# Kernel tuning notes

Hardware: AMD Instinct MI355X
Metric: run time of the kernel (lower is better)

## Reference

```python
import jax, jax.numpy as jnp
import numpy as np
from jax import lax

# Per-tensor power-of-two scales (ScalingImplType.CONST / POWER_OF_TWO in Brevitas)
S_ACT8 = 2.0 ** -4   # 8-bit signed input quant scale
S_ACT4 = 2.0 ** -1   # 4-bit signed input quant scale
S_W = 2.0 ** -2      # per-tensor weight quant scale
S_RELU = 2.0 ** -2   # 4-bit unsigned QuantReLU scale


def fq(x, scale, qmin, qmax):
    # fake-quant with straight-through estimator (STE)
    q = jnp.clip(jnp.round(x / scale), qmin, qmax) * scale
    return x + lax.stop_gradient(q - x)


def fq_signed(x, scale, bits):
    return fq(x, scale, -(2 ** (bits - 1)), 2 ** (bits - 1) - 1)


def fq_uint(x, scale, bits):
    return fq(x, scale, 0, 2 ** bits - 1)


def qconv(x, w, in_bits, w_bits, s_in, stride=1, padding=0, groups=1):
    xq = fq_signed(x, s_in, in_bits)
    wq = fq_signed(w, S_W, w_bits)
    return lax.conv_general_dilated(
        xq, wq, (stride, stride), [(padding, padding)] * 2,
        feature_group_count=groups,
        dimension_numbers=('NCHW', 'OIHW', 'NCHW'))


def maxpool(x, k, s):
    return lax.reduce_window(x, -jnp.inf, lax.max,
                             (1, 1, k, k), (1, 1, s, s), 'VALID')


def dwsep(x, dw, pw):
    c = x.shape[1]
    x = qconv(x, dw, 4, 4, S_ACT4, padding=1, groups=c)  # depthwise 3x3
    x = qconv(x, pw, 4, 4, S_ACT4)                       # pointwise 1x1
    return x


def qrelu4(x):
    return fq_uint(jax.nn.relu(x), S_RELU, 4)


def setup_inputs() -> dict:
    key = jax.random.key(0)
    ks = jax.random.split(key, 10)
    B = 1024
    mk = lambda k, shp, sc=0.5: jax.random.normal(k, shp, jnp.float32) * sc
    return {
        'x': jax.random.normal(ks[0], (B, 3, 32, 32), jnp.float32),
        'w0': mk(ks[1], (3, 3, 1, 1)),
        'dw1': mk(ks[2], (3, 1, 3, 3)),
        'pw1': mk(ks[3], (32, 3, 1, 1)),
        'dw2': mk(ks[4], (32, 1, 3, 3)),
        'pw2': mk(ks[5], (64, 32, 1, 1)),
        'dw3': mk(ks[6], (64, 1, 3, 3)),
        'pw3': mk(ks[7], (128, 64, 1, 1)),
        'wc1': mk(ks[8], (256, 128, 1, 1)),
        'wc2': mk(ks[9], (10, 256, 1, 1)),
    }


def reference(x, w0, dw1, pw1, dw2, pw2, dw3, pw3, wc1, wc2):
    # features
    h = qconv(x, w0, 8, 8, S_ACT8)            # 1x1, 3->3, 8-bit
    h = dwsep(h, dw1, pw1)                    # 3->32, 32x32
    h = qrelu4(h)
    h = maxpool(h, 2, 2)                      # 16x16
    h = dwsep(h, dw2, pw2)                    # 32->64
    h = qrelu4(h)
    h = maxpool(h, 2, 2)                      # 8x8
    h = dwsep(h, dw3, pw3)                    # 64->128
    h = qrelu4(h)
    h = maxpool(h, 8, 1)                      # 1x1
    # classifier
    h = qconv(h, wc1, 4, 4, S_ACT4)           # 128->256
    h = qrelu4(h)
    h = qconv(h, wc2, 4, 4, S_ACT4)           # 256->10
    h = fq_signed(h, S_ACT8, 8)               # output quant int8
    return h
```

## Files before the change

### kernel.cpp

```cpp
#include <hip/hip_runtime.h>

#define W0i   0
#define DW1i  9
#define PW1i  36
#define DW2i  132
#define DW3i  420
#define PW2p  996
#define PW3p  1508
#define WC1p  3556
#define WC2p  11748
#define WTOT  12388

__device__ __forceinline__ int iclamp(int v, int lo, int hi) {
  return v < lo ? lo : (v > hi ? hi : v);
}

__device__ __forceinline__ int rne4(int a) {
  return (a + 1 + ((a >> 2) & 1)) >> 2;
}
__device__ __forceinline__ int rne32(int a) {
  return (a + 15 + ((a >> 5) & 1)) >> 5;
}

__device__ __forceinline__ int dot4(int a, int b, int c) {
#if defined(__has_builtin)
#if __has_builtin(__builtin_amdgcn_sdot4)
  return __builtin_amdgcn_sdot4(a, b, c, false);
#else
  c += ((a << 24) >> 24) * ((b << 24) >> 24);
  c += ((a << 16) >> 24) * ((b << 16) >> 24);
  c += ((a <<  8) >> 24) * ((b <<  8) >> 24);
  c += (a >> 24) * (b >> 24);
  return c;
#endif
#else
  c += ((a << 24) >> 24) * ((b << 24) >> 24);
  c += ((a << 16) >> 24) * ((b << 16) >> 24);
  c += ((a <<  8) >> 24) * ((b <<  8) >> 24);
  c += (a >> 24) * (b >> 24);
  return c;
#endif
}

__device__ __forceinline__ int alignb(int hi, int lo, int sh) {
#if defined(__has_builtin)
#if __has_builtin(__builtin_amdgcn_alignbyte)
  return __builtin_amdgcn_alignbyte(hi, lo, sh);
#else
  return (int)(((((unsigned long long)(unsigned)hi) << 32) |
                (unsigned)lo) >> (8 * sh));
#endif
#else
  return (int)(((((unsigned long long)(unsigned)hi) << 32) |
                (unsigned)lo) >> (8 * sh));
#endif
}

__device__ __forceinline__ int pack3(int a, int b, int c) {
  return (a & 0xff) | ((b & 0xff) << 8) | ((c & 0xff) << 16);
}

__global__ __launch_bounds__(256) void prep_weights(
    const float* __restrict__ w0,  const float* __restrict__ dw1,
    const float* __restrict__ pw1, const float* __restrict__ dw2,
    const float* __restrict__ pw2, const float* __restrict__ dw3,
    const float* __restrict__ pw3, const float* __restrict__ wc1,
    const float* __restrict__ wc2, int* __restrict__ ws) {
  int t = blockIdx.x * blockDim.x + threadIdx.x;
  if (t >= WTOT) return;
  if (t < PW2p) {
    float w; int lo = -8, hi = 7;
    if (t < DW1i)      { w = w0[t];        lo = -128; hi = 127; }
    else if (t < PW1i)   w = dw1[t - DW1i];
    else if (t < DW2i)   w = pw1[t - PW1i];
    else if (t < DW3i)   w = dw2[t - DW2i];
    else                 w = dw3[t - DW3i];
    ws[t] = iclamp((int)rintf(w * 4.f), lo, hi);
  } else {
    const float* src;
    if (t < WC1p) {
      if (t < PW3p) src = pw2 + (t - PW2p) * 4;
      else          src = pw3 + (t - PW3p) * 4;
    } else {
      if (t < WC2p) src = wc1 + (t - WC1p) * 4;
      else          src = wc2 + (t - WC2p) * 4;
    }
    int p = 0;
#pragma unroll
    for (int b = 0; b < 4; b++) {
      int c = iclamp((int)rintf(src[b] * 4.f), -8, 7);
      p |= (c & 0xff) << (8 * b);
    }
    ws[t] = p;
  }
}

__global__ __launch_bounds__(256, 4) void fused_net(
    const float* __restrict__ x,
    const int*   __restrict__ wq,
    float* __restrict__ out)
{
  const int img = blockIdx.x;
  const int tid = threadIdx.x;

  __shared__ __align__(16) int bufAi[2384];
  __shared__ __align__(16) int bufBi[2592];
  __shared__ int s_red[256];

  {
    const float* xim = x + (size_t)img * 3072;
    const int p4 = tid * 4;
    float4 v0 = *(const float4*)(xim + p4);
    float4 v1 = *(const float4*)(xim + 1024 + p4);
    float4 v2 = *(const float4*)(xim + 2048 + p4);
    int w[9];
#pragma unroll
    for (int i = 0; i < 9; i++) w[i] = wq[W0i + i];
#define Q8(v) iclamp((int)rintf((v) * 16.f), -128, 127)
    int a0[4] = {Q8(v0.x), Q8(v0.y), Q8(v0.z), Q8(v0.w)};
    int a1[4] = {Q8(v1.x), Q8(v1.y), Q8(v1.z), Q8(v1.w)};
    int a2[4] = {Q8(v2.x), Q8(v2.y), Q8(v2.z), Q8(v2.w)};
#undef Q8
#pragma unroll
    for (int o = 0; o < 3; o++) {
      int pk = 0;
#pragma unroll
      for (int j = 0; j < 4; j++) {
        int s = a0[j] * w[o * 3] + a1[j] * w[o * 3 + 1] + a2[j] * w[o * 3 + 2];
        pk |= (iclamp(rne32(s), -8, 7) & 0xff) << (8 * j);
      }
      bufAi[o * 256 + tid] = pk;
    }
  }
  __syncthreads();

  {
    const int y = tid >> 3, q = tid & 7;
#pragma unroll
    for (int c = 0; c < 3; c++) {
      int wr[3];
#pragma unroll
      for (int r = 0; r < 3; r++)
        wr[r] = pack3(wq[DW1i + c * 9 + r * 3], wq[DW1i + c * 9 + r * 3 + 1],
                      wq[DW1i + c * 9 + r * 3 + 2]);
      const int* ap = bufAi + c * 256;
      int acc0 = 0, acc1 = 0, acc2 = 0, acc3 = 0;
#pragma unroll
      for (int ky = 0; ky < 3; ky++) {
        int yy = y + ky - 1;
        if (yy < 0 || yy > 31) continue;
        int base = yy * 8 + q;
        int dC = ap[base];
        int dL = q ? ap[base - 1] : 0;
        int dR = (q < 7) ? ap[base + 1] : 0;
        int w = wr[ky];
        acc0 = dot4(alignb(dC, dL, 3), w, acc0);
        acc1 = dot4(dC, w, acc1);
        acc2 = dot4(alignb(dR, dC, 1), w, acc2);
        acc3 = dot4(alignb(dR, dC, 2), w, acc3);
      }
      int pk = (iclamp(rne4(acc0), -8, 7) & 0xff) |
               ((iclamp(rne4(acc1), -8, 7) & 0xff) << 8) |
               ((iclamp(rne4(acc2), -8, 7) & 0xff) << 16) |
               ((iclamp(rne4(acc3), -8, 7) & 0xff) << 24);
      bufBi[c * 256 + tid] = pk;
    }
  }
  __syncthreads();

  {
    const int py = tid >> 4, px = tid & 15;
    const signed char* bB = (const signed char*)bufBi;
    int a[4];
#pragma unroll
    for (int d = 0; d < 4; d++) {
      int sp = (2 * py + (d >> 1)) * 32 + 2 * px + (d & 1);
      a[d] = pack3(bB[sp], bB[1024 + sp], bB[2048 + sp]);
    }
#pragma unroll
    for (int it = 0; it < 8; it++) {
      int pk = 0;
#pragma unroll
      for (int j = 0; j < 4; j++) {
        int o = it * 4 + j;
        int wpk = pack3(wq[PW1i + o * 3], wq[PW1i + o * 3 + 1],
                        wq[PW1i + o * 3 + 2]);
        int m0 = dot4(a[0], wpk, 0), m1 = dot4(a[1], wpk, 0);
        int m2 = dot4(a[2], wpk, 0), m3 = dot4(a[3], wpk, 0);
        int mx = max(max(m0, m1), max(m2, m3));
        pk |= iclamp(rne4(mx), 0, 7) << (8 * j);
      }
      bufAi[py * 149 + px * 9 + it] = pk;
    }
  }
  __syncthreads();

  for (int it2 = 0; it2 < 2; it2++) {
    int idx = tid + 256 * it2;
    int cq = __builtin_amdgcn_readfirstlane(idx >> 6);
    int s = idx & 63;
    int y = s >> 2, x0 = (s & 3) << 2;
    int wk[9][4];
#pragma unroll
    for (int t9 = 0; t9 < 9; t9++)
#pragma unroll
      for (int cc = 0; cc < 4; cc++)
        wk[t9][cc] = wq[DW2i + (cq * 4 + cc) * 9 + t9];
    int acc[4][4] = {};
#pragma unroll
    for (int ky = 0; ky < 3; ky++) {
      int yy = y + ky - 1;
      if (yy < 0 || yy > 15) continue;
      int rb = yy * 149 + cq;
      int rd[6];
      rd[0] = (x0 > 0) ? bufAi[rb + (x0 - 1) * 9] : 0;
      rd[1] = bufAi[rb + x0 * 9];
      rd[2] = bufAi[rb + (x0 + 1) * 9];
      rd[3] = bufAi[rb + (x0 + 2) * 9];
      rd[4] = bufAi[rb + (x0 + 3) * 9];
      rd[5] = (x0 < 12) ? bufAi[rb + (x0 + 4) * 9] : 0;
      int e[6][4];
#pragma unroll
      for (int k = 0; k < 6; k++)
#pragma unroll
        for (int cc = 0; cc < 4; cc++) e[k][cc] = (rd[k] >> (8 * cc)) & 0xf;
#pragma unroll
      for (int j = 0; j < 4; j++)
#pragma unroll
        for (int kx = 0; kx < 3; kx++)
#pragma unroll
          for (int cc = 0; cc < 4; cc++)
            acc[j][cc] += e[j + kx][cc] * wk[ky * 3 + kx][cc];
    }
#pragma unroll
    for (int j = 0; j < 4; j++) {
      int pk = 0;
#pragma unroll
      for (int cc = 0; cc < 4; cc++)
        pk |= (iclamp(rne4(acc[j][cc]), -8, 7) & 0xff) << (8 * cc);
      bufBi[y * 162 + (x0 + j) * 10 + cq] = pk;
    }
  }
  __syncthreads();

  {
    int oq = tid & 15;
    int4 w4[4][2];
#pragma unroll
    for (int j = 0; j < 4; j++) {
      const int4* wp = (const int4*)(wq + PW2p + (oq * 4 + j) * 8);
      w4[j][0] = wp[0]; w4[j][1] = wp[1];
    }
    for (int it = 0; it < 4; it++) {
      int pp = (tid >> 4) + 16 * it;
      int py = pp >> 3, px = pp & 7;
      int mx[4] = {-1000000, -1000000, -1000000, -1000000};
#pragma unroll
      for (int d = 0; d < 4; d++) {
        int sy = 2 * py + (d >> 1), sx = 2 * px + (d & 1);
        const int2* ap = (const int2*)(bufBi + sy * 162 + sx * 10);
        int2 A0 = ap[0], A1 = ap[1], A2 = ap[2], A3 = ap[3];
#pragma unroll
        for (int j = 0; j < 4; j++) {
          int acc = dot4(A0.x, w4[j][0].x, 0);
          acc = dot4(A0.y, w4[j][0].y, acc);
          acc = dot4(A1.x, w4[j][0].z, acc);
          acc = dot4(A1.y, w4[j][0].w, acc);
          acc = dot4(A2.x, w4[j][1].x, acc);
          acc = dot4(A2.y, w4[j][1].y, acc);
          acc = dot4(A3.x, w4[j][1].z, acc);
          acc = dot4(A3.y, w4[j][1].w, acc);
          mx[j] = mx[j] > acc ? mx[j] : acc;
        }
      }
      int pk = 0;
#pragma unroll
      for (int j = 0; j < 4; j++)
        pk |= iclamp(rne4(mx[j]), 0, 7) << (8 * j);
      bufAi[py * 137 + px * 17 + oq] = pk;
    }
  }
  __syncthreads();

  {
    int cq2 = tid >> 4;
    int s = tid & 15;
    int y = s >> 1, x0 = (s & 1) << 2;
    int wk[9][4];
#pragma unroll
    for (int t9 = 0; t9 < 9; t9++)
#pragma unroll
      for (int cc = 0; cc < 4; cc++)
        wk[t9][cc] = wq[DW3i + (cq2 * 4 + cc) * 9 + t9];
    int acc[4][4] = {};
#pragma unroll
    for (int ky = 0; ky < 3; ky++) {
      int yy = y + ky - 1;
      if (yy < 0 || yy > 7) continue;
      int rb = yy * 137 + cq2;
      int rd[6];
      rd[0] = (x0 == 4) ? bufAi[rb + (x0 - 1) * 17] : 0;
      rd[1] = bufAi[rb + x0 * 17];
      rd[2] = bufAi[rb + (x0 + 1) * 17];
      rd[3] = bufAi[rb + (x0 + 2) * 17];
      rd[4] = bufAi[rb + (x0 + 3) * 17];
      rd[5] = (x0 == 0) ? bufAi[rb + (x0 + 4) * 17] : 0;
      int e[6][4];
#pragma unroll
      for (int k = 0; k < 6; k++)
#pragma unroll
        for (int cc = 0; cc < 4; cc++) e[k][cc] = (rd[k] >> (8 * cc)) & 0xf;
#pragma unroll
      for (int j = 0; j < 4; j++)
#pragma unroll
        for (int kx = 0; kx < 3; kx++)
#pragma unroll
          for (int cc = 0; cc < 4; cc++)
            acc[j][cc] += e[j + kx][cc] * wk[ky * 3 + kx][cc];
    }
#pragma unroll
    for (int j = 0; j < 4; j++) {
      int pk = 0;
#pragma unroll
      for (int cc = 0; cc < 4; cc++)
        pk |= (iclamp(rne4(acc[j][cc]), -8, 7) & 0xff) << (8 * cc);
      bufBi[y * 164 + (x0 + j) * 20 + cq2] = pk;
    }
  }
  __syncthreads();

  {
    int o = tid >> 1, half = tid & 1;
    const int4* wp = (const int4*)(wq + PW3p + o * 16);
    int4 w0v = wp[0], w1v = wp[1], w2v = wp[2], w3v = wp[3];
    int mx = -1000000;
    for (int k = 0; k < 32; k++) {
      int sp = half + 2 * k;
      int py = sp >> 3, px = sp & 7;
      const int4* ap = (const int4*)(bufBi + py * 164 + px * 20);
      int4 A0 = ap[0], A1 = ap[1], A2 = ap[2], A3 = ap[3];
      int acc = dot4(A0.x, w0v.x, 0);
      acc = dot4(A0.y, w0v.y, acc); acc = dot4(A0.z, w0v.z, acc);
      acc = dot4(A0.w, w0v.w, acc);
      acc = dot4(A1.x, w1v.x, acc); acc = dot4(A1.y, w1v.y, acc);
      acc = dot4(A1.z, w1v.z, acc); acc = dot4(A1.w, w1v.w, acc);
      acc = dot4(A2.x, w2v.x, acc); acc = dot4(A2.y, w2v.y, acc);
      acc = dot4(A2.z, w2v.z, acc); acc = dot4(A2.w, w2v.w, acc);
      acc = dot4(A3.x, w3v.x, acc); acc = dot4(A3.y, w3v.y, acc);
      acc = dot4(A3.z, w3v.z, acc); acc = dot4(A3.w, w3v.w, acc);
      mx = mx > acc ? mx : acc;
    }
    s_red[tid] = mx;
  }
  __syncthreads();
  if (tid < 128) {
    int mm = s_red[2 * tid] > s_red[2 * tid + 1] ? s_red[2 * tid]
                                                 : s_red[2 * tid + 1];
    ((signed char*)bufAi)[tid] = (signed char)iclamp(rne4(mm), 0, 7);
  }
  __syncthreads();

  {
    const int4* wp = (const int4*)(wq + WC1p + tid * 32);
    const int4* mp = (const int4*)bufAi;
    int acc = 0;
#pragma unroll
    for (int rI = 0; rI < 8; rI++) {
      int4 a = mp[rI]; int4 w = wp[rI];
      acc = dot4(a.x, w.x, acc); acc = dot4(a.y, w.y, acc);
      acc = dot4(a.z, w.z, acc); acc = dot4(a.w, w.w, acc);
    }
    ((signed char*)bufBi)[tid] = (signed char)iclamp(rne4(acc), 0, 7);
  }
  __syncthreads();

  if (tid < 80) {
    int k = tid >> 3, j = tid & 7;
    const int4* wp = (const int4*)(wq + WC2p + k * 64 + j * 8);
    int4 w0v = wp[0], w1v = wp[1];
    const int4* ap = (const int4*)bufBi;
    int4 A0 = ap[j * 2], A1 = ap[j * 2 + 1];
    int acc = dot4(A0.x, w0v.x, 0);
    acc = dot4(A0.y, w0v.y, acc); acc = dot4(A0.z, w0v.z, acc);
    acc = dot4(A0.w, w0v.w, acc);
    acc = dot4(A1.x, w1v.x, acc); acc = dot4(A1.y, w1v.y, acc);
    acc = dot4(A1.z, w1v.z, acc); acc = dot4(A1.w, w1v.w, acc);
    s_red[tid] = acc;
  }
  __syncthreads();
  if (tid < 10) {
    int acc = 0;
#pragma unroll
    for (int j = 0; j < 8; j++) acc += s_red[tid * 8 + j];
    int code = iclamp(2 * acc, -128, 127);
    out[(size_t)img * 10 + tid] = (float)code * 0.0625f;
  }
}

extern "C" void kernel_launch(void* const* d_in, const int* in_sizes, int n_in,
                              void* d_out, int out_size, void* d_ws, size_t ws_size,
                              hipStream_t stream) {
  const float* x   = (const float*)d_in[0];
  const float* w0  = (const float*)d_in[1];
  const float* dw1 = (const float*)d_in[2];
  const float* pw1 = (const float*)d_in[3];
  const float* dw2 = (const float*)d_in[4];
  const float* pw2 = (const float*)d_in[5];
  const float* dw3 = (const float*)d_in[6];
  const float* pw3 = (const float*)d_in[7];
  const float* wc1 = (const float*)d_in[8];
  const float* wc2 = (const float*)d_in[9];
  int*   wsq = (int*)d_ws;
  float* out = (float*)d_out;

  prep_weights<<<(WTOT + 255) / 256, 256, 0, stream>>>(
      w0, dw1, pw1, dw2, pw2, dw3, pw3, wc1, wc2, wsq);
  fused_net<<<1024, 256, 0, stream>>>(x, wsq, out);
}
```

Baseline: 105.9 us.

## Use MFMA int8 matrix instructions for pointwise convs pw2 and pw3

Replaces the sdot4-based pointwise 1x1 convolutions in stages 2 and 3 with __builtin_amdgcn_mfma_i32_16x16x32_i8. The prep kernel adds pre-swizzled weight fragments in MFMA B-operand layout, and activations are regathered in shared memory so each 2x2 maxpool window falls inside one MFMA tile. Pooling then becomes a max over accumulator lanes plus cross-lane shuffles. This cuts the VALU dot-product work, at the cost of an extra LDS gather pass, more shared memory and different buffer ping-ponging that could cause bank conflicts or reduce occupancy.

```diff
diff --git a/kernel.cpp b/kernel.cpp
--- a/kernel.cpp
+++ b/kernel.cpp
@@ -1,4 +1,6 @@
 #include <hip/hip_runtime.h>
+
+typedef int v4i __attribute__((ext_vector_type(4)));
 
 #define W0i   0
 #define DW1i  9
@@ -9,12 +11,13 @@
 #define PW3p  1508
 #define WC1p  3556
 #define WC2p  11748
-#define WTOT  12388
+#define PW2Fb 12388
+#define PW3Fb 12900
+#define WTOT  14948
 
 __device__ __forceinline__ int iclamp(int v, int lo, int hi) {
   return v < lo ? lo : (v > hi ? hi : v);
 }
-
 __device__ __forceinline__ int rne4(int a) {
   return (a + 1 + ((a >> 2) & 1)) >> 2;
 }
@@ -23,8 +26,7 @@
 }
 
 __device__ __forceinline__ int dot4(int a, int b, int c) {
-#if defined(__has_builtin)
-#if __has_builtin(__builtin_amdgcn_sdot4)
+#if defined(__has_builtin) && __has_builtin(__builtin_amdgcn_sdot4)
   return __builtin_amdgcn_sdot4(a, b, c, false);
 #else
   c += ((a << 24) >> 24) * ((b << 24) >> 24);
@@ -33,23 +35,11 @@
   c += (a >> 24) * (b >> 24);
   return c;
 #endif
-#else
-  c += ((a << 24) >> 24) * ((b << 24) >> 24);
-  c += ((a << 16) >> 24) * ((b << 16) >> 24);
-  c += ((a <<  8) >> 24) * ((b <<  8) >> 24);
-  c += (a >> 24) * (b >> 24);
-  return c;
-#endif
 }
 
 __device__ __forceinline__ int alignb(int hi, int lo, int sh) {
-#if defined(__has_builtin)
-#if __has_builtin(__builtin_amdgcn_alignbyte)
+#if defined(__has_builtin) && __has_builtin(__builtin_amdgcn_alignbyte)
   return __builtin_amdgcn_alignbyte(hi, lo, sh);
-#else
-  return (int)(((((unsigned long long)(unsigned)hi) << 32) |
-                (unsigned)lo) >> (8 * sh));
-#endif
 #else
   return (int)(((((unsigned long long)(unsigned)hi) << 32) |
                 (unsigned)lo) >> (8 * sh));
@@ -76,7 +66,7 @@
     else if (t < DW3i)   w = dw2[t - DW2i];
     else                 w = dw3[t - DW3i];
     ws[t] = iclamp((int)rintf(w * 4.f), lo, hi);
-  } else {
+  } else if (t < PW2Fb) {
     const float* src;
     if (t < WC1p) {
       if (t < PW3p) src = pw2 + (t - PW2p) * 4;
@@ -92,6 +82,31 @@
       p |= (c & 0xff) << (8 * b);
     }
     ws[t] = p;
+  } else if (t < PW3Fb) {
+    int i = t - PW2Fb;
+    int nt = i >> 7, r = i & 127, lane = r >> 1, dw = r & 1;
+    int n = nt * 16 + (lane & 15);
+    int kb = (lane >> 4) * 8 + dw * 4;
+    int p = 0;
+#pragma unroll
+    for (int b = 0; b < 4; b++) {
+      int c = iclamp((int)rintf(pw2[n * 32 + kb + b] * 4.f), -8, 7);
+      p |= (c & 0xff) << (8 * b);
+    }
+    ws[t] = p;
+  } else {
+    int i = t - PW3Fb;
+    int g = i >> 7, r = i & 127, lane = r >> 1, dw = r & 1;
+    int nt = g >> 1, kh = g & 1;
+    int n = nt * 16 + (lane & 15);
+    int kb = kh * 32 + (lane >> 4) * 8 + dw * 4;
+    int p = 0;
+#pragma unroll
+    for (int b = 0; b < 4; b++) {
+      int c = iclamp((int)rintf(pw3[n * 64 + kb + b] * 4.f), -8, 7);
+      p |= (c & 0xff) << (8 * b);
+    }
+    ws[t] = p;
   }
 }
 
@@ -103,7 +118,7 @@
   const int img = blockIdx.x;
   const int tid = threadIdx.x;
 
-  __shared__ __align__(16) int bufAi[2384];
+  __shared__ __align__(16) int bufAi[2560];
   __shared__ __align__(16) int bufBi[2592];
   __shared__ int s_red[256];
 
@@ -243,41 +258,36 @@
   }
   __syncthreads();
 
-  {
-    int oq = tid & 15;
-    int4 w4[4][2];
-#pragma unroll
-    for (int j = 0; j < 4; j++) {
-      const int4* wp = (const int4*)(wq + PW2p + (oq * 4 + j) * 8);
-      w4[j][0] = wp[0]; w4[j][1] = wp[1];
-    }
-    for (int it = 0; it < 4; it++) {
-      int pp = (tid >> 4) + 16 * it;
-      int py = pp >> 3, px = pp & 7;
-      int mx[4] = {-1000000, -1000000, -1000000, -1000000};
-#pragma unroll
-      for (int d = 0; d < 4; d++) {
-        int sy = 2 * py + (d >> 1), sx = 2 * px + (d & 1);
-        const int2* ap = (const int2*)(bufBi + sy * 162 + sx * 10);
-        int2 A0 = ap[0], A1 = ap[1], A2 = ap[2], A3 = ap[3];
-#pragma unroll
-        for (int j = 0; j < 4; j++) {
-          int acc = dot4(A0.x, w4[j][0].x, 0);
-          acc = dot4(A0.y, w4[j][0].y, acc);
-          acc = dot4(A1.x, w4[j][0].z, acc);
-          acc = dot4(A1.y, w4[j][0].w, acc);
-          acc = dot4(A2.x, w4[j][1].x, acc);
-          acc = dot4(A2.y, w4[j][1].y, acc);
-          acc = dot4(A3.x, w4[j][1].z, acc);
-          acc = dot4(A3.y, w4[j][1].w, acc);
-          mx[j] = mx[j] > acc ? mx[j] : acc;
-        }
-      }
-      int pk = 0;
-#pragma unroll
-      for (int j = 0; j < 4; j++)
-        pk |= iclamp(rne4(mx[j]), 0, 7) << (8 * j);
-      bufAi[py * 137 + px * 17 + oq] = pk;
+#pragma unroll
+  for (int i = 0; i < 4; i++) {
+    int id = tid + 256 * i;
+    int m = id >> 2, c2 = id & 3;
+    int qp = m >> 2, d = m & 3;
+    int sy = ((qp >> 3) << 1) + (d >> 1);
+    int sx = ((qp & 7) << 1) + (d & 1);
+    long v = *(const long*)(bufBi + sy * 162 + sx * 10 + c2 * 2);
+    *(long*)(bufAi + m * 10 + c2 * 2) = v;
+  }
+  __syncthreads();
+
+  {
+    const int w = tid >> 6, lane = tid & 63;
+    const int lm = lane & 15, kg = lane >> 4;
+    const long bw = *(const long*)(wq + PW2Fb + (w * 64 + lane) * 2);
+    const signed char* Ab = (const signed char*)bufAi;
+    signed char* A2c = (signed char*)bufBi;
+    const int n = w * 16 + lm;
+#pragma unroll 4
+    for (int mt = 0; mt < 16; mt++) {
+      int m = mt * 16 + lm;
+      long av = *(const long*)(Ab + m * 40 + kg * 8);
+      v4i d = __builtin_amdgcn_mfma_i32_16x16x32_i8(av, bw, (v4i){0, 0, 0, 0},
+                                                    0, 0, 0);
+      int mx = max(max(d[0], d[1]), max(d[2], d[3]));
+      int qp = mt * 4 + kg;
+      int py = qp >> 3, px = qp & 7;
+      A2c[(py * 137 + px * 17 + (n >> 2)) * 4 + (n & 3)] =
+          (signed char)iclamp(rne4(mx), 0, 7);
     }
   }
   __syncthreads();
@@ -299,12 +309,12 @@
       if (yy < 0 || yy > 7) continue;
       int rb = yy * 137 + cq2;
       int rd[6];
-      rd[0] = (x0 == 4) ? bufAi[rb + (x0 - 1) * 17] : 0;
-      rd[1] = bufAi[rb + x0 * 17];
-      rd[2] = bufAi[rb + (x0 + 1) * 17];
-      rd[3] = bufAi[rb + (x0 + 2) * 17];
-      rd[4] = bufAi[rb + (x0 + 3) * 17];
-      rd[5] = (x0 == 0) ? bufAi[rb + (x0 + 4) * 17] : 0;
+      rd[0] = (x0 == 4) ? bufBi[rb + (x0 - 1) * 17] : 0;
+      rd[1] = bufBi[rb + x0 * 17];
+      rd[2] = bufBi[rb + (x0 + 1) * 17];
+      rd[3] = bufBi[rb + (x0 + 2) * 17];
+      rd[4] = bufBi[rb + (x0 + 3) * 17];
+      rd[5] = (x0 == 0) ? bufBi[rb + (x0 + 4) * 17] : 0;
       int e[6][4];
 #pragma unroll
       for (int k = 0; k < 6; k++)
@@ -324,45 +334,44 @@
 #pragma unroll
       for (int cc = 0; cc < 4; cc++)
         pk |= (iclamp(rne4(acc[j][cc]), -8, 7) & 0xff) << (8 * cc);
-      bufBi[y * 164 + (x0 + j) * 20 + cq2] = pk;
-    }
-  }
-  __syncthreads();
-
-  {
-    int o = tid >> 1, half = tid & 1;
-    const int4* wp = (const int4*)(wq + PW3p + o * 16);
-    int4 w0v = wp[0], w1v = wp[1], w2v = wp[2], w3v = wp[3];
-    int mx = -1000000;
-    for (int k = 0; k < 32; k++) {
-      int sp = half + 2 * k;
-      int py = sp >> 3, px = sp & 7;
-      const int4* ap = (const int4*)(bufBi + py * 164 + px * 20);
-      int4 A0 = ap[0], A1 = ap[1], A2 = ap[2], A3 = ap[3];
-      int acc = dot4(A0.x, w0v.x, 0);
-      acc = dot4(A0.y, w0v.y, acc); acc = dot4(A0.z, w0v.z, acc);
-      acc = dot4(A0.w, w0v.w, acc);
-      acc = dot4(A1.x, w1v.x, acc); acc = dot4(A1.y, w1v.y, acc);
-      acc = dot4(A1.z, w1v.z, acc); acc = dot4(A1.w, w1v.w, acc);
-      acc = dot4(A2.x, w2v.x, acc); acc = dot4(A2.y, w2v.y, acc);
-      acc = dot4(A2.z, w2v.z, acc); acc = dot4(A2.w, w2v.w, acc);
-      acc = dot4(A3.x, w3v.x, acc); acc = dot4(A3.y, w3v.y, acc);
-      acc = dot4(A3.z, w3v.z, acc); acc = dot4(A3.w, w3v.w, acc);
-      mx = mx > acc ? mx : acc;
-    }
-    s_red[tid] = mx;
-  }
-  __syncthreads();
-  if (tid < 128) {
-    int mm = s_red[2 * tid] > s_red[2 * tid + 1] ? s_red[2 * tid]
-                                                 : s_red[2 * tid + 1];
-    ((signed char*)bufAi)[tid] = (signed char)iclamp(rne4(mm), 0, 7);
+      bufAi[(y * 8 + x0 + j) * 18 + cq2] = pk;
+    }
+  }
+  __syncthreads();
+
+  {
+    const int w = tid >> 6, lane = tid & 63;
+    const int lm = lane & 15, kg = lane >> 4;
+    const signed char* Ab = (const signed char*)bufAi;
+    signed char* fcin = (signed char*)bufBi;
+#pragma unroll
+    for (int h = 0; h < 2; h++) {
+      int nt = w * 2 + h;
+      const long b0 = *(const long*)(wq + PW3Fb + (nt * 2 + 0) * 128 + lane * 2);
+      const long b1 = *(const long*)(wq + PW3Fb + (nt * 2 + 1) * 128 + lane * 2);
+      int mx = -1000000;
+#pragma unroll
+      for (int mt = 0; mt < 4; mt++) {
+        int m = mt * 16 + lm;
+        long a0 = *(const long*)(Ab + m * 72 + kg * 8);
+        long a1 = *(const long*)(Ab + m * 72 + 32 + kg * 8);
+        v4i d = __builtin_amdgcn_mfma_i32_16x16x32_i8(a0, b0, (v4i){0, 0, 0, 0},
+                                                      0, 0, 0);
+        d = __builtin_amdgcn_mfma_i32_16x16x32_i8(a1, b1, d, 0, 0, 0);
+        int t4 = max(max(d[0], d[1]), max(d[2], d[3]));
+        mx = mx > t4 ? mx : t4;
+      }
+      mx = max(mx, __shfl_xor(mx, 16));
+      mx = max(mx, __shfl_xor(mx, 32));
+      if (lane < 16)
+        fcin[nt * 16 + lm] = (signed char)iclamp(rne4(mx), 0, 7);
+    }
   }
   __syncthreads();
 
   {
     const int4* wp = (const int4*)(wq + WC1p + tid * 32);
-    const int4* mp = (const int4*)bufAi;
+    const int4* mp = (const int4*)bufBi;
     int acc = 0;
 #pragma unroll
     for (int rI = 0; rI < 8; rI++) {
@@ -370,7 +379,7 @@
       acc = dot4(a.x, w.x, acc); acc = dot4(a.y, w.y, acc);
       acc = dot4(a.z, w.z, acc); acc = dot4(a.w, w.w, acc);
     }
-    ((signed char*)bufBi)[tid] = (signed char)iclamp(rne4(acc), 0, 7);
+    ((signed char*)bufAi)[tid] = (signed char)iclamp(rne4(acc), 0, 7);
   }
   __syncthreads();
 
@@ -378,7 +387,7 @@
     int k = tid >> 3, j = tid & 7;
     const int4* wp = (const int4*)(wq + WC2p + k * 64 + j * 8);
     int4 w0v = wp[0], w1v = wp[1];
-    const int4* ap = (const int4*)bufBi;
+    const int4* ap = (const int4*)bufAi;
     int4 A0 = ap[j * 2], A1 = ap[j * 2 + 1];
     int acc = dot4(A0.x, w0v.x, 0);
     acc = dot4(A0.y, w0v.y, acc); acc = dot4(A0.z, w0v.z, acc);
```

Result: faster. 97.88 us (-7.6%).
